# Kernel tuning notes

Measured on AMD Instinct MI355X. Metric: run time of the kernel, lower is better.

Reference implementation:

```python
import jax, jax.numpy as jnp
import numpy as np

IN_DIM = 128
OUT_DIM = 128
NUM_INTERVALS = 8
SPLINE_ORDER = 3
BATCH = 1024


def make_grids():
    # domain [-1, 1] for every (in, out) pair, extended by spline_order knots each side
    step = 2.0 / NUM_INTERVALS
    G = NUM_INTERVALS + 2 * SPLINE_ORDER + 1
    g = (-1.0 - SPLINE_ORDER * step) + jnp.arange(G, dtype=jnp.float32) * step  # [G]
    return jnp.broadcast_to(g, (IN_DIM, OUT_DIM, G))


def setup_inputs() -> dict:
    key = jax.random.key(0)
    k1, k2, k3 = jax.random.split(key, 3)
    x = jax.random.normal(k1, (BATCH, IN_DIM), dtype=jnp.float32)
    n_cp = NUM_INTERVALS + SPLINE_ORDER
    control_points = 0.1 * jax.random.normal(k2, (IN_DIM, OUT_DIM, n_cp), dtype=jnp.float32)
    scaling_factors = np.sqrt(2.0 / OUT_DIM).astype(np.float32) * jax.random.normal(
        k3, (IN_DIM, OUT_DIM), dtype=jnp.float32)
    grids = make_grids()
    return {"x": x, "control_points": control_points,
            "scaling_factors": scaling_factors, "grids": grids}


def bspline_bases(x, grids, k):
    # Bottom-up Cox-de-Boor DP (identical recurrence to the naive top-down version).
    # x: [B, in], grids: [in, out, G] -> returns all degree-k bases [B, in, out, G-1-k]
    ex = x[:, :, None, None]          # [B, in, 1, 1]
    t = grids[None]                   # [1, in, out, G]
    B = ((t[..., :-1] <= ex) & (ex < t[..., 1:])).astype(x.dtype)  # degree 0
    for d in range(1, k + 1):
        tl  = t[..., : -(d + 1)]      # t[i]
        tr  = t[..., d:-1]            # t[i+d]
        tl1 = t[..., 1:-d]            # t[i+1]
        tr1 = t[..., d + 1:]          # t[i+d+1]
        B = (ex - tl) / (tr - tl) * B[..., :-1] + (tr1 - ex) / (tr1 - tl1) * B[..., 1:]
    return B


def reference(x, control_points, scaling_factors, grids):
    Bk = bspline_bases(x, grids, SPLINE_ORDER)                 # [B, in, out, n_cp]
    spline = jnp.einsum('biog,iog->bio', Bk, control_points)    # [B, in, out]
    res = scaling_factors[None] * (jax.nn.silu(x)[:, :, None] + spline)
    return jnp.sum(res, axis=1).astype(jnp.float32)             # [B, out]
```

## Files before the change

kernel.cpp:

```cpp
#include <hip/hip_runtime.h>
#include <math.h>


#define IN_DIM   128
#define OUT_DIM  128
#define NCP      11
#define FS       12
#define KTOT     (IN_DIM * FS)
#define KCH      96
#define NCHUNK   (KTOT / KCH)
#define MT       64
#define STEPS    (KCH / 32)
#define PSU      104

typedef __attribute__((ext_vector_type(8))) short short8;
typedef __attribute__((ext_vector_type(4))) float f32x4;

static __device__ __forceinline__ unsigned short f2bf(float f) {
    unsigned int x = __float_as_uint(f);
    unsigned int r = (x + 0x7fffu + ((x >> 16) & 1u)) >> 16;
    return (unsigned short)r;
}

__global__ __launch_bounds__(256)
void kan_prep(const float* __restrict__ CP, const float* __restrict__ SF,
              unsigned short* __restrict__ Wz)
{
    const int idx  = blockIdx.x * 256 + threadIdx.x;
    const int s    = idx >> 9;
    const int rem  = idx & 511;
    const int t    = rem >> 6;
    const int lane = rem & 63;
    const int o     = 16 * t + (lane & 15);
    const int kbase = 32 * s + 8 * (lane >> 4);

    unsigned int q[4];
    #pragma unroll
    for (int jj = 0; jj < 4; ++jj) {
        unsigned short lo, hi;
        #pragma unroll
        for (int half = 0; half < 2; ++half) {
            const int k = kbase + 2 * jj + half;
            const int i = k / 12;
            const int g = k - 12 * i;
            const float sf = SF[i * OUT_DIM + o];
            const float v  = (g == NCP) ? sf : sf * CP[(i * OUT_DIM + o) * NCP + g];
            if (half == 0) lo = f2bf(v); else hi = f2bf(v);
        }
        q[jj] = (unsigned int)lo | ((unsigned int)hi << 16);
    }
    *(uint4*)&Wz[idx * 8] = make_uint4(q[0], q[1], q[2], q[3]);
}

__global__ __launch_bounds__(256)
void kan_gemm(const float* __restrict__ X, const float* __restrict__ GR,
              const unsigned short* __restrict__ Wz, float* __restrict__ P,
              int M)
{
    __shared__ __align__(16) unsigned short A[MT * PSU];

    const int tid = threadIdx.x;
    const int m0  = blockIdx.x * MT;
    const int c   = blockIdx.y;
    const int i0  = 8 * c;

    const float t0   = GR[0];
    const float invh = 1.0f / (GR[1] - t0);

    #pragma unroll
    for (int kq = 0; kq < 2; ++kq) {
        const int p_ = tid + kq * 256;
        const int r  = p_ >> 3;
        const int il = p_ & 7;
        const int i  = i0 + il;

        const float x  = X[(m0 + r) * IN_DIM + i];
        const float xr = (x - t0) * invh;
        const float pf = floorf(xr);
        const int   p  = (int)pf;
        const float u  = xr - pf;
        const float um = 1.0f - u;
        const float u2 = u * u, u3 = u2 * u;
        const float c0 = um * um * um * (1.0f / 6.0f);
        const float c1 = (3.0f * u3 - 6.0f * u2 + 4.0f) * (1.0f / 6.0f);
        const float c2 = (-3.0f * u3 + 3.0f * u2 + 3.0f * u + 1.0f) * (1.0f / 6.0f);
        const float c3 = u3 * (1.0f / 6.0f);
        const float silu = x / (1.0f + __expf(-x));

        const bool ok = (p >= 0) && (p <= 13);
        const int  j0 = ok ? (p - 3) : -999;
        const int  pp = ok ? p : -999;

        unsigned short us[12];
        #pragma unroll
        for (int g = 0; g < NCP; ++g) {
            float v = (g == j0)     ? c0
                    : (g == j0 + 1) ? c1
                    : (g == j0 + 2) ? c2
                    : (g == pp)     ? c3 : 0.0f;
            us[g] = f2bf(v);
        }
        us[NCP] = f2bf(silu);

        uint2* dst = (uint2*)&A[r * PSU + il * FS];
        dst[0] = make_uint2((unsigned)us[0] | ((unsigned)us[1] << 16),
                            (unsigned)us[2] | ((unsigned)us[3] << 16));
        dst[1] = make_uint2((unsigned)us[4] | ((unsigned)us[5] << 16),
                            (unsigned)us[6] | ((unsigned)us[7] << 16));
        dst[2] = make_uint2((unsigned)us[8] | ((unsigned)us[9] << 16),
                            (unsigned)us[10] | ((unsigned)us[11] << 16));
    }
    __syncthreads();

    const int lane = tid & 63;
    const int w    = tid >> 6;
    const int row  = lane & 15;
    const int quad = lane >> 4;

    f32x4 acc[8];
    #pragma unroll
    for (int t = 0; t < 8; ++t) acc[t] = (f32x4){0.f, 0.f, 0.f, 0.f};

    const unsigned short* abase = &A[(16 * w + row) * PSU];
    #pragma unroll
    for (int s = 0; s < STEPS; ++s) {
        const short8 a = *(const short8*)(abase + s * 32 + 8 * quad);
        const int sg = STEPS * c + s;
        const unsigned short* bb = Wz + (size_t)((sg * 8) * 64 + lane) * 8;
        #pragma unroll
        for (int t = 0; t < 8; ++t) {
            const short8 b = *(const short8*)(bb + (size_t)t * 64 * 8);
            acc[t] = __builtin_amdgcn_mfma_f32_16x16x32_bf16(a, b, acc[t], 0, 0, 0);
        }
    }

    float* Pc = P + (size_t)c * M * OUT_DIM;
    #pragma unroll
    for (int t = 0; t < 8; ++t) {
        #pragma unroll
        for (int q = 0; q < 4; ++q) {
            const int rr = m0 + 16 * w + quad * 4 + q;
            Pc[rr * OUT_DIM + 16 * t + row] = acc[t][q];
        }
    }
}

__global__ __launch_bounds__(256)
void kan_reduce(const float* __restrict__ P, float* __restrict__ OUT, int M)
{
    const int e = blockIdx.x * 256 + threadIdx.x;
    float v = 0.0f;
    #pragma unroll
    for (int c = 0; c < NCHUNK; ++c)
        v += P[(size_t)c * M * OUT_DIM + e];
    OUT[e] = v;
}

extern "C" void kernel_launch(void* const* d_in, const int* in_sizes, int n_in,
                              void* d_out, int out_size, void* d_ws, size_t ws_size,
                              hipStream_t stream) {
    const float* x  = (const float*)d_in[0];
    const float* cp = (const float*)d_in[1];
    const float* sf = (const float*)d_in[2];
    const float* gr = (const float*)d_in[3];
    float* out = (float*)d_out;

    const int batch = in_sizes[0] / IN_DIM;

    unsigned short* Wz = (unsigned short*)d_ws;
    float* P = (float*)((char*)d_ws + (size_t)KTOT * OUT_DIM * 2);

    kan_prep<<<(KTOT / 32) * 8 * 64 / 256, 256, 0, stream>>>(cp, sf, Wz);
    dim3 grid(batch / MT, NCHUNK);
    kan_gemm<<<grid, 256, 0, stream>>>(x, gr, Wz, P, batch);
    kan_reduce<<<batch * OUT_DIM / 256, 256, 0, stream>>>(P, out, batch);
}
```

Baseline: 71.10 us.

## Replace split-K GEMM plus reduce with full-K GEMM over 16-row tiles

The GEMM no longer splits the 1536-long K dimension into 16 chunks that write fp32 partials and need a separate reduction kernel. Each block now takes 16 batch rows and the whole K range, and each wave computes two 16-column output tiles that are written straight to the output. This removes the partial-sum traffic and one kernel launch. In exchange the grid shrinks to 64 blocks, each running a longer serial MFMA loop, and every block re-reads all of the B weights.

```diff
diff --git a/kernel.cpp b/kernel.cpp
--- a/kernel.cpp
+++ b/kernel.cpp
@@ -7,11 +7,9 @@
 #define NCP      11
 #define FS       12
 #define KTOT     (IN_DIM * FS)
-#define KCH      96
-#define NCHUNK   (KTOT / KCH)
-#define MT       64
-#define STEPS    (KCH / 32)
-#define PSU      104
+#define MT       16
+#define NSTEP    (KTOT / 32)
+#define ASTR     1544
 
 typedef __attribute__((ext_vector_type(8))) short short8;
 typedef __attribute__((ext_vector_type(4))) float f32x4;
@@ -37,7 +35,7 @@
     unsigned int q[4];
     #pragma unroll
     for (int jj = 0; jj < 4; ++jj) {
-        unsigned short lo, hi;
+        unsigned short lo = 0, hi = 0;
         #pragma unroll
         for (int half = 0; half < 2; ++half) {
             const int k = kbase + 2 * jj + half;
@@ -54,25 +52,21 @@
 
 __global__ __launch_bounds__(256)
 void kan_gemm(const float* __restrict__ X, const float* __restrict__ GR,
-              const unsigned short* __restrict__ Wz, float* __restrict__ P,
-              int M)
+              const unsigned short* __restrict__ Wz, float* __restrict__ OUT)
 {
-    __shared__ __align__(16) unsigned short A[MT * PSU];
+    __shared__ __align__(16) unsigned short A[MT * ASTR];
 
     const int tid = threadIdx.x;
     const int m0  = blockIdx.x * MT;
-    const int c   = blockIdx.y;
-    const int i0  = 8 * c;
 
     const float t0   = GR[0];
     const float invh = 1.0f / (GR[1] - t0);
 
     #pragma unroll
-    for (int kq = 0; kq < 2; ++kq) {
+    for (int kq = 0; kq < (MT * IN_DIM) / 256; ++kq) {
         const int p_ = tid + kq * 256;
-        const int r  = p_ >> 3;
-        const int il = p_ & 7;
-        const int i  = i0 + il;
+        const int r  = p_ >> 7;
+        const int i  = p_ & (IN_DIM - 1);
 
         const float x  = X[(m0 + r) * IN_DIM + i];
         const float xr = (x - t0) * invh;
@@ -91,7 +85,7 @@
         const int  j0 = ok ? (p - 3) : -999;
         const int  pp = ok ? p : -999;
 
-        unsigned short us[12];
+        unsigned short us[FS];
         #pragma unroll
         for (int g = 0; g < NCP; ++g) {
             float v = (g == j0)     ? c0
@@ -102,7 +96,7 @@
         }
         us[NCP] = f2bf(silu);
 
-        uint2* dst = (uint2*)&A[r * PSU + il * FS];
+        uint2* dst = (uint2*)&A[r * ASTR + i * FS];
         dst[0] = make_uint2((unsigned)us[0] | ((unsigned)us[1] << 16),
                             (unsigned)us[2] | ((unsigned)us[3] << 16));
         dst[1] = make_uint2((unsigned)us[4] | ((unsigned)us[5] << 16),
@@ -117,43 +111,26 @@
     const int row  = lane & 15;
     const int quad = lane >> 4;
 
-    f32x4 acc[8];
-    #pragma unroll
-    for (int t = 0; t < 8; ++t) acc[t] = (f32x4){0.f, 0.f, 0.f, 0.f};
+    f32x4 acc0 = (f32x4){0.f, 0.f, 0.f, 0.f};
+    f32x4 acc1 = (f32x4){0.f, 0.f, 0.f, 0.f};
 
-    const unsigned short* abase = &A[(16 * w + row) * PSU];
-    #pragma unroll
-    for (int s = 0; s < STEPS; ++s) {
-        const short8 a = *(const short8*)(abase + s * 32 + 8 * quad);
-        const int sg = STEPS * c + s;
-        const unsigned short* bb = Wz + (size_t)((sg * 8) * 64 + lane) * 8;
-        #pragma unroll
-        for (int t = 0; t < 8; ++t) {
-            const short8 b = *(const short8*)(bb + (size_t)t * 64 * 8);
-            acc[t] = __builtin_amdgcn_mfma_f32_16x16x32_bf16(a, b, acc[t], 0, 0, 0);
-        }
+    const unsigned short* ab = &A[row * ASTR];
+    #pragma unroll 8
+    for (int s = 0; s < NSTEP; ++s) {
+        const short8 a  = *(const short8*)(ab + s * 32 + 8 * quad);
+        const unsigned short* b = Wz + (size_t)((s * 8 + 2 * w) * 64 + lane) * 8;
+        const short8 bA = *(const short8*)(b);
+        const short8 bB = *(const short8*)(b + 64 * 8);
+        acc0 = __builtin_amdgcn_mfma_f32_16x16x32_bf16(a, bA, acc0, 0, 0, 0);
+        acc1 = __builtin_amdgcn_mfma_f32_16x16x32_bf16(a, bB, acc1, 0, 0, 0);
     }
 
-    float* Pc = P + (size_t)c * M * OUT_DIM;
     #pragma unroll
-    for (int t = 0; t < 8; ++t) {
-        #pragma unroll
-        for (int q = 0; q < 4; ++q) {
-            const int rr = m0 + 16 * w + quad * 4 + q;
-            Pc[rr * OUT_DIM + 16 * t + row] = acc[t][q];
-        }
+    for (int q = 0; q < 4; ++q) {
+        const int rr = m0 + 4 * quad + q;
+        OUT[rr * OUT_DIM + 16 * (2 * w + 0) + row] = acc0[q];
+        OUT[rr * OUT_DIM + 16 * (2 * w + 1) + row] = acc1[q];
     }
-}
-
-__global__ __launch_bounds__(256)
-void kan_reduce(const float* __restrict__ P, float* __restrict__ OUT, int M)
-{
-    const int e = blockIdx.x * 256 + threadIdx.x;
-    float v = 0.0f;
-    #pragma unroll
-    for (int c = 0; c < NCHUNK; ++c)
-        v += P[(size_t)c * M * OUT_DIM + e];
-    OUT[e] = v;
 }
 
 extern "C" void kernel_launch(void* const* d_in, const int* in_sizes, int n_in,
@@ -168,10 +145,7 @@
     const int batch = in_sizes[0] / IN_DIM;
 
     unsigned short* Wz = (unsigned short*)d_ws;
-    float* P = (float*)((char*)d_ws + (size_t)KTOT * OUT_DIM * 2);
 
-    kan_prep<<<(KTOT / 32) * 8 * 64 / 256, 256, 0, stream>>>(cp, sf, Wz);
-    dim3 grid(batch / MT, NCHUNK);
-    kan_gemm<<<grid, 256, 0, stream>>>(x, gr, Wz, P, batch);
-    kan_reduce<<<batch * OUT_DIM / 256, 256, 0, stream>>>(P, out, batch);
+    kan_prep<<<(NSTEP * 8 * 64) / 256, 256, 0, stream>>>(cp, sf, Wz);
+    kan_gemm<<<batch / MT, 256, 0, stream>>>(x, gr, Wz, out);
 }
```

Result: slower. 79.68 us (+12.1%).
